# Optimization experiments

Hardware: AMD Instinct MI355X
Metric: run time of the kernel (lower is better)

## Reference

```python
import jax, jax.numpy as jnp
import numpy as np
from jax import lax

B, SEQ, ENC_IN, PRED = 16, 512, 321, 96
DM, DSTATE, DCONV, EXPAND, ELAYERS = 512, 16, 4, 2, 2
DI = EXPAND * DM            # 1024
DTRANK = -(-DM // 16)       # 32
EPS = 1e-5
NMAMBA = 2                  # mamba1/mamba2 shared across all encoder layers


def setup_inputs() -> dict:
    key = jax.random.key(0)
    ks = jax.random.split(key, 10)
    nrm = lambda k, sh, s=0.02: jax.random.normal(k, sh, dtype=jnp.float32) * s
    return {
        "x": jax.random.normal(ks[0], (B, SEQ, ENC_IN), dtype=jnp.float32),
        "revin_w": jnp.ones((ENC_IN,), jnp.float32),
        "revin_b": jnp.zeros((ENC_IN,), jnp.float32),
        "lin1_w": nrm(ks[1], (DM, SEQ)),
        "lin1_b": jnp.zeros((DM,), jnp.float32),
        "head_w": nrm(ks[2], (PRED, DM)),
        "head_b": jnp.zeros((PRED,), jnp.float32),
        "in_proj_w": nrm(ks[3], (NMAMBA, 2 * DI, DM)),
        "conv_w": nrm(ks[4], (NMAMBA, DI, DCONV), 0.1),
        "conv_b": jnp.zeros((NMAMBA, DI), jnp.float32),
        "x_proj_w": nrm(ks[5], (NMAMBA, DTRANK + 2 * DSTATE, DI)),
        "dt_proj_w": nrm(ks[6], (NMAMBA, DI, DTRANK), 0.1),
        "dt_proj_b": nrm(ks[7], (NMAMBA, DI), 0.1),
        "A_log": jnp.log(jnp.broadcast_to(jnp.arange(1, DSTATE + 1, dtype=jnp.float32), (NMAMBA, DI, DSTATE))),
        "D": jnp.ones((NMAMBA, DI), jnp.float32),
        "out_proj_w": nrm(ks[8], (NMAMBA, DM, DI)),
    }


def _mamba(x, ipw, cw, cb, xpw, dpw, dpb, A_log, Dp, opw):
    # x: (B, L, DM) -> (B, L, DM); standard Mamba selective-scan block
    xz = jnp.einsum('bld,ed->ble', x, ipw)            # (B,L,2*DI)
    xr, z = jnp.split(xz, 2, axis=-1)
    # causal depthwise conv over token axis L
    k = cw.T[:, None, :]                              # (DCONV,1,DI)
    xc = lax.conv_general_dilated(xr, k, window_strides=(1,), padding=[(DCONV - 1, 0)],
                                  dimension_numbers=('NHC', 'HIO', 'NHC'), feature_group_count=DI)
    xc = jax.nn.silu(xc + cb)
    dbl = jnp.einsum('bld,ed->ble', xc, xpw)          # (B,L,DTRANK+2N)
    dt, Bm, Cm = jnp.split(dbl, [DTRANK, DTRANK + DSTATE], axis=-1)
    delta = jax.nn.softplus(jnp.einsum('blr,dr->bld', dt, dpw) + dpb)  # (B,L,DI)
    A = -jnp.exp(A_log)                               # (DI,N)

    def step(h, xs):
        d_t, B_t, C_t, x_t = xs                       # (B,DI),(B,N),(B,N),(B,DI)
        dA = jnp.exp(d_t[..., None] * A)              # (B,DI,N)
        h = dA * h + (d_t * x_t)[..., None] * B_t[:, None, :]
        y = jnp.einsum('bdn,bn->bd', h, C_t)
        return h, y

    h0 = jnp.zeros((x.shape[0], DI, DSTATE), x.dtype)
    xs = (delta.transpose(1, 0, 2), Bm.transpose(1, 0, 2), Cm.transpose(1, 0, 2), xc.transpose(1, 0, 2))
    _, ys = lax.scan(step, h0, xs)
    y = ys.transpose(1, 0, 2) + Dp * xc
    y = y * jax.nn.silu(z)
    return jnp.einsum('bld,ed->ble', y, opw)


def reference(x, revin_w, revin_b, lin1_w, lin1_b, head_w, head_b,
              in_proj_w, conv_w, conv_b, x_proj_w, dt_proj_w, dt_proj_b,
              A_log, D, out_proj_w):
    # RevIN normalize (stats over time dim)
    mean = x.mean(1, keepdims=True)
    std = jnp.sqrt(x.var(1, keepdims=True) + EPS)
    xn = (x - mean) / std * revin_w + revin_b
    # channels become tokens; embed lookback window
    t = xn.transpose(0, 2, 1)                         # (B, ENC_IN, SEQ)
    t = t @ lin1_w.T + lin1_b                         # (B, ENC_IN, DM)
    p = lambda i: (in_proj_w[i], conv_w[i], conv_b[i], x_proj_w[i],
                   dt_proj_w[i], dt_proj_b[i], A_log[i], D[i], out_proj_w[i])
    for _ in range(ELAYERS):                          # mamba1/mamba2 weights shared across layers
        fwd = _mamba(t, *p(0))
        bwd = jnp.flip(_mamba(jnp.flip(t, 1), *p(1)), 1)   # is_flip bidirectional branch
        t = fwd + bwd + t
    out = t @ head_w.T + head_b                       # (B, ENC_IN, PRED)
    out = out.transpose(0, 2, 1)                      # (B, PRED, ENC_IN)
    # RevIN denorm
    out = (out - revin_b) / (revin_w + EPS * EPS)
    out = out * std + mean
    return out
```

## Files before the change

kernel.cpp:

```cpp
#include <hip/hip_runtime.h>
#include <hip/hip_bf16.h>
#include <cstdint>
#include <cstddef>

#define B_    16
#define SEQ_  512
#define CIN_  321
#define PRED_ 96
#define DM_   512
#define DI_   1024
#define NST_  16
#define RNK_  32
#define L_    321
#define NT_   (B_*CIN_)
#define PADM_ 5248
#define TC_   41
#define NC_   8
#define PS_   384

typedef unsigned short ushort_t;
typedef __bf16 bf16x8 __attribute__((ext_vector_type(8)));
typedef float  f32x4  __attribute__((ext_vector_type(4)));
typedef __attribute__((address_space(3))) void lds_void_t;
typedef const __attribute__((address_space(1))) void gbl_void_t;

__device__ __forceinline__ float sigmoidf_(float x){ return 1.f/(1.f+__expf(-x)); }
__device__ __forceinline__ float softplusf_(float x){
    return (x > 15.f) ? x : __logf(1.f + __expf(x));
}
__device__ __forceinline__ ushort_t f2bf(float f){
    union { float f; unsigned u; } v; v.f = f;
    unsigned r = v.u + 0x7FFF + ((v.u >> 16) & 1);
    return (ushort_t)(r >> 16);
}
__device__ __forceinline__ float bf2f(ushort_t u){
    return __uint_as_float(((unsigned)u) << 16);
}

struct EpiBiasDual {
    float* C; ushort_t* Cb; const float* bias;
    __device__ void operator()(int z, int m, int n, float v) const {
        float o = v + bias[n];
        C[(size_t)m*DM_ + n] = o;
        Cb[(size_t)m*DM_ + n] = f2bf(o);
    }
};
struct EpiXZ {
    ushort_t* xzb;
    __device__ void operator()(int z, int m, int n, float v) const {
        int mm = m;
        if (z) { int b = m / L_; int l = m - b*L_; mm = b*L_ + (L_-1 - l); }
        xzb[(size_t)z*PADM_*2*DI_ + (size_t)mm*(2*DI_) + n] = f2bf(v);
    }
};
struct EpiDbl {
    float* C; ushort_t* dtb;
    __device__ void operator()(int z, int m, int n, float v) const {
        if (n < 32)
            dtb[(size_t)z*PADM_*32 + (size_t)m*32 + n] = f2bf(v);
        else if (n < 64)
            C[(size_t)z*NT_*64 + (size_t)m*64 + n] = v;
    }
};
struct EpiSpB {
    ushort_t* C; const float* bias;
    __device__ void operator()(int z, int m, int n, float v) const {
        C[(size_t)z*NT_*DI_ + (size_t)m*DI_ + n] = f2bf(softplusf_(v + bias[z*DI_ + n]));
    }
};
struct EpiP {
    float* P;
    __device__ void operator()(int z, int m, int n, float v) const {
        P[(size_t)z*NT_*DM_ + (size_t)m*DM_ + n] = v;
    }
};
struct EpiHead {
    float* out; const float* bias; const float* mean; const float* stdv;
    const float* rw; const float* rb;
    __device__ void operator()(int z, int m, int n, float v) const {
        int b = m / CIN_, c = m - b*CIN_;
        float o = v + bias[n];
        o = (o - rb[c]) / (rw[c] + 1e-10f);
        o = o * stdv[m] + mean[m];
        out[((size_t)b*PRED_ + n)*CIN_ + c] = o;
    }
};

template<int BK, typename Epi>
__global__ __launch_bounds__(256) void gemm_bf16(const ushort_t* __restrict__ A, int lda, size_t zsa,
                                                 const ushort_t* __restrict__ Bw, int ldb, size_t zsb,
                                                 int M, int N, int K, Epi epi)
{
    __shared__ __align__(16) ushort_t As[128*BK];
    __shared__ __align__(16) ushort_t Bs[128*BK];
    const int z = blockIdx.z;
    A += (size_t)z*zsa; Bw += (size_t)z*zsb;
    const int tid  = threadIdx.x;
    const int m0 = blockIdx.x * 128, n0 = blockIdx.y * 128;
    const int wave = tid >> 6, lane = tid & 63;
    const int wm = (wave & 1) * 64, wn = (wave >> 1) * 64;
    const int ln16 = lane & 15, quad = lane >> 4;

    f32x4 acc[4][4] = {};

    if (BK == 64) {
        const int r8 = lane >> 3;
        const int colg = ((lane & 7) ^ r8) * 8;
        const ushort_t* Ag = A + (size_t)(m0 + wave*32 + r8)*lda + colg;
        const ushort_t* Bg = Bw + (size_t)(n0 + wave*32 + r8)*ldb + colg;
        ushort_t* AsW = As + wave*32*64;
        ushort_t* BsW = Bs + wave*32*64;
        for (int k0 = 0; k0 < K; k0 += 64) {
            #pragma unroll
            for (int j = 0; j < 4; ++j) {
                __builtin_amdgcn_global_load_lds((gbl_void_t*)(Ag + k0 + (size_t)(j*8)*lda),
                                                 (lds_void_t*)(AsW + j*8*64), 16, 0, 0);
                __builtin_amdgcn_global_load_lds((gbl_void_t*)(Bg + k0 + (size_t)(j*8)*ldb),
                                                 (lds_void_t*)(BsW + j*8*64), 16, 0, 0);
            }
            __syncthreads();
            #pragma unroll
            for (int ks = 0; ks < 2; ++ks) {
                bf16x8 af[4], bfr[4];
                #pragma unroll
                for (int i = 0; i < 4; ++i) {
                    int ra = wm + i*16 + ln16;
                    af[i]  = *(const bf16x8*)(As + ra*64 + (((ks*4 + quad) ^ (ra & 7)) * 8));
                    int rb2 = wn + i*16 + ln16;
                    bfr[i] = *(const bf16x8*)(Bs + rb2*64 + (((ks*4 + quad) ^ (rb2 & 7)) * 8));
                }
                #pragma unroll
                for (int mi = 0; mi < 4; ++mi)
                    #pragma unroll
                    for (int ni = 0; ni < 4; ++ni)
                        acc[mi][ni] = __builtin_amdgcn_mfma_f32_16x16x32_bf16(af[mi], bfr[ni], acc[mi][ni], 0, 0, 0);
            }
            __syncthreads();
        }
    } else {
        const int srow = lane >> 2, scol = (lane & 3) * 8;
        const ushort_t* Ag = A + (size_t)(m0 + wave*32 + srow)*lda + scol;
        const ushort_t* Bg = Bw + (size_t)(n0 + wave*32 + srow)*ldb + scol;
        ushort_t* AsW = As + wave*32*32;
        ushort_t* BsW = Bs + wave*32*32;
        for (int k0 = 0; k0 < K; k0 += 32) {
            __builtin_amdgcn_global_load_lds((gbl_void_t*)(Ag + k0),                  (lds_void_t*)AsW,           16, 0, 0);
            __builtin_amdgcn_global_load_lds((gbl_void_t*)(Ag + k0 + 16*(size_t)lda), (lds_void_t*)(AsW + 16*32), 16, 0, 0);
            __builtin_amdgcn_global_load_lds((gbl_void_t*)(Bg + k0),                  (lds_void_t*)BsW,           16, 0, 0);
            __builtin_amdgcn_global_load_lds((gbl_void_t*)(Bg + k0 + 16*(size_t)ldb), (lds_void_t*)(BsW + 16*32), 16, 0, 0);
            __syncthreads();
            bf16x8 af[4], bfr[4];
            #pragma unroll
            for (int i = 0; i < 4; ++i)
                af[i] = *(const bf16x8*)(As + (wm + i*16 + ln16)*32 + quad*8);
            #pragma unroll
            for (int i = 0; i < 4; ++i)
                bfr[i] = *(const bf16x8*)(Bs + (wn + i*16 + ln16)*32 + quad*8);
            #pragma unroll
            for (int mi = 0; mi < 4; ++mi)
                #pragma unroll
                for (int ni = 0; ni < 4; ++ni)
                    acc[mi][ni] = __builtin_amdgcn_mfma_f32_16x16x32_bf16(af[mi], bfr[ni], acc[mi][ni], 0, 0, 0);
            __syncthreads();
        }
    }

    #pragma unroll
    for (int mi = 0; mi < 4; ++mi) {
        #pragma unroll
        for (int r = 0; r < 4; ++r) {
            int m = m0 + wm + mi*16 + quad*4 + r;
            if (m >= M) continue;
            #pragma unroll
            for (int ni = 0; ni < 4; ++ni) {
                int n = n0 + wn + ni*16 + ln16;
                if (n < N) epi(z, m, n, acc[mi][ni][r]);
            }
        }
    }
}

struct CvtArgs {
    const float* src[7];
    ushort_t*    dst[7];
    int n4[7];
    int start[8];
};
__global__ __launch_bounds__(256) void cvt_all(CvtArgs a)
{
    int bid = blockIdx.x;
    int seg = 0;
    #pragma unroll
    for (int i = 0; i < 6; ++i) seg += (bid >= a.start[i+1]) ? 1 : 0;
    int idx = (bid - a.start[seg])*256 + threadIdx.x;
    if (idx < a.n4[seg]) {
        float4 v = ((const float4*)a.src[seg])[idx];
        ushort4 u; u.x=f2bf(v.x); u.y=f2bf(v.y); u.z=f2bf(v.z); u.w=f2bf(v.w);
        ((ushort4*)a.dst[seg])[idx] = u;
    }
}

__global__ __launch_bounds__(256) void revin_partial(const float* __restrict__ x,
                                                     float* __restrict__ psum,
                                                     float* __restrict__ psq)
{
    int b = blockIdx.x;
    int c0 = blockIdx.y * 64;
    int sz = blockIdx.z;
    int cl = threadIdx.x & 63;
    int sl = threadIdx.x >> 6;
    int c = c0 + cl;
    int s0 = sz * 64;
    float sum = 0.f, sq = 0.f;
    if (c < CIN_) {
        #pragma unroll
        for (int i = 0; i < 16; ++i) {
            int s = s0 + sl + i*4;
            float v = x[((size_t)b*SEQ_ + s)*CIN_ + c];
            sum += v; sq += v*v;
        }
    }
    __shared__ float ssum[4][64], ssq[4][64];
    ssum[sl][cl] = sum; ssq[sl][cl] = sq;
    __syncthreads();
    if (sl == 0 && c < CIN_) {
        float s = ssum[0][cl]+ssum[1][cl]+ssum[2][cl]+ssum[3][cl];
        float q = ssq[0][cl]+ssq[1][cl]+ssq[2][cl]+ssq[3][cl];
        psum[((size_t)b*8 + sz)*PS_ + c] = s;
        psq [((size_t)b*8 + sz)*PS_ + c] = q;
    }
}
__global__ __launch_bounds__(384) void revin_final(const float* __restrict__ psum,
                                                   const float* __restrict__ psq,
                                                   float* __restrict__ meanb,
                                                   float* __restrict__ stdb)
{
    int b = blockIdx.x;
    int c = threadIdx.x;
    if (c >= CIN_) return;
    float s = 0.f, q = 0.f;
    #pragma unroll
    for (int i = 0; i < 8; ++i) {
        s += psum[((size_t)b*8 + i)*PS_ + c];
        q += psq [((size_t)b*8 + i)*PS_ + c];
    }
    float mn = s * (1.f/SEQ_);
    float var = q * (1.f/SEQ_) - mn*mn;
    meanb[b*CIN_ + c] = mn;
    stdb[b*CIN_ + c]  = sqrtf(var + 1e-5f);
}

__global__ __launch_bounds__(256) void norm_transpose(const float* __restrict__ x,
                                                      const float* __restrict__ meanb,
                                                      const float* __restrict__ stdb,
                                                      const float* __restrict__ rw,
                                                      const float* __restrict__ rb,
                                                      ushort_t* __restrict__ xt)
{
    __shared__ float tile[64][65];
    int b = blockIdx.x, s0 = blockIdx.y*64, c0 = blockIdx.z*64;
    int cl = threadIdx.x & 63, sl = threadIdx.x >> 6;
    #pragma unroll
    for (int i = 0; i < 16; ++i) {
        int s = s0 + sl + i*4;
        int c = c0 + cl;
        float v = 0.f;
        if (c < CIN_) v = x[((size_t)b*SEQ_ + s)*CIN_ + c];
        tile[sl + i*4][cl] = v;
    }
    __syncthreads();
    int sl2 = threadIdx.x & 63, cl2 = threadIdx.x >> 6;
    #pragma unroll
    for (int i = 0; i < 16; ++i) {
        int c = c0 + cl2 + i*4;
        if (c >= CIN_) continue;
        int m = b*CIN_ + c;
        float v = tile[sl2][cl2 + i*4];
        v = (v - meanb[m]) / stdb[m] * rw[c] + rb[c];
        xt[(size_t)m*SEQ_ + s0 + sl2] = f2bf(v);
    }
}

__global__ __launch_bounds__(256) void conv_silu(const ushort_t* __restrict__ xzb,
                                                 const float* __restrict__ cw,
                                                 const float* __restrict__ cb,
                                                 ushort_t* __restrict__ xcb)
{
    int m = blockIdx.x;
    int d = blockIdx.y*256 + threadIdx.x;
    int im = blockIdx.z;
    const ushort_t* xz = xzb + (size_t)im*PADM_*2*DI_;
    int b = m / L_, l = m - b*L_;
    float4 w = ((const float4*)cw)[(size_t)im*DI_ + d];
    float wv[4] = {w.x, w.y, w.z, w.w};
    float a = cb[im*DI_ + d];
    #pragma unroll
    for (int j = 0; j < 4; ++j) {
        int ls = l - 3 + j;
        if (ls >= 0) a += bf2f(xz[((size_t)(b*L_ + ls))*(2*DI_) + d]) * wv[j];
    }
    float o = a * sigmoidf_(a);
    xcb[(size_t)im*PADM_*DI_ + (size_t)m*DI_ + d] = f2bf(o);
}

#define SCAN_LOADS(tok)                                                          \
    float dv = bf2f(dlz[(size_t)(tok)*DI_ + d]);                                 \
    float xv = bf2f(xcz[(size_t)(tok)*DI_ + d]);                                 \
    float4 B0 = *(const float4*)(dbz + (size_t)(tok)*64 + 32);                   \
    float4 B1 = *(const float4*)(dbz + (size_t)(tok)*64 + 36);                   \
    float4 B2 = *(const float4*)(dbz + (size_t)(tok)*64 + 40);                   \
    float4 B3 = *(const float4*)(dbz + (size_t)(tok)*64 + 44);                   \
    float Bv[16] = {B0.x,B0.y,B0.z,B0.w, B1.x,B1.y,B1.z,B1.w,                    \
                    B2.x,B2.y,B2.z,B2.w, B3.x,B3.y,B3.z,B3.w};

__global__ __launch_bounds__(64, 1) void scan_p1(const ushort_t* __restrict__ dl,
                                                 const ushort_t* __restrict__ xcb,
                                                 const float* __restrict__ dbl,
                                                 const float* __restrict__ A_log,
                                                 float* __restrict__ hloc,
                                                 float* __restrict__ Ssum)
{
    const int im = blockIdx.z >> 4, b = blockIdx.z & 15;
    const int c = blockIdx.y;
    const int d = blockIdx.x*64 + threadIdx.x;
    const ushort_t* dlz = dl + (size_t)im*NT_*DI_;
    const ushort_t* xcz = xcb + (size_t)im*PADM_*DI_;
    const float* dbz = dbl + (size_t)im*NT_*64;
    float a[NST_];
    #pragma unroll
    for (int n = 0; n < NST_; ++n)
        a[n] = -__expf(A_log[((size_t)im*DI_ + d)*NST_ + n]);
    bool uni = true;
    #pragma unroll
    for (int n = 1; n < NST_; ++n)
        uni = uni && (fabsf(a[n] - (n+1)*a[0]) <= 1e-3f*(n+1));
    const float a0 = a[0];
    const int t0 = c*TC_, tend = (t0 + TC_ < L_) ? t0 + TC_ : L_;
    float h[NST_] = {};
    float S = 0.f;
    if (uni) {
        for (int t = t0; t < tend; ++t) {
            int tok = b*L_ + t;
            SCAN_LOADS(tok)
            S += dv;
            float du = dv * xv;
            float e1 = __expf(dv * a0), dAn = e1;
            #pragma unroll
            for (int n = 0; n < NST_; ++n) { h[n] = dAn*h[n] + du*Bv[n]; dAn *= e1; }
        }
    } else {
        for (int t = t0; t < tend; ++t) {
            int tok = b*L_ + t;
            SCAN_LOADS(tok)
            S += dv;
            float du = dv * xv;
            #pragma unroll
            for (int n = 0; n < NST_; ++n) h[n] = __expf(dv*a[n])*h[n] + du*Bv[n];
        }
    }
    size_t base = ((size_t)(im*16 + b)*NC_ + c);
    Ssum[base*DI_ + d] = S;
    #pragma unroll
    for (int n = 0; n < NST_; ++n)
        hloc[(base*NST_ + n)*DI_ + d] = h[n];
}

__global__ __launch_bounds__(64, 1) void scan_compose(const float* __restrict__ A_log,
                                                      float* __restrict__ hloc,
                                                      const float* __restrict__ Ssum)
{
    const int im = blockIdx.z >> 4, b = blockIdx.z & 15;
    const int d = blockIdx.x*64 + threadIdx.x;
    float a[NST_];
    #pragma unroll
    for (int n = 0; n < NST_; ++n)
        a[n] = -__expf(A_log[((size_t)im*DI_ + d)*NST_ + n]);
    float carry[NST_] = {};
    for (int c = 0; c < NC_; ++c) {
        size_t base = ((size_t)(im*16 + b)*NC_ + c);
        float S = Ssum[base*DI_ + d];
        #pragma unroll
        for (int n = 0; n < NST_; ++n) {
            size_t idx = (base*NST_ + n)*DI_ + d;
            float hl = hloc[idx];
            hloc[idx] = carry[n];
            carry[n] = __expf(a[n]*S)*carry[n] + hl;
        }
    }
}

__global__ __launch_bounds__(64, 1) void scan_p2(const ushort_t* __restrict__ dl,
                                                 const ushort_t* __restrict__ xcb,
                                                 ushort_t* __restrict__ xzb,
                                                 const float* __restrict__ dbl,
                                                 const float* __restrict__ A_log,
                                                 const float* __restrict__ Dp,
                                                 const float* __restrict__ hloc)
{
    const int im = blockIdx.z >> 4, b = blockIdx.z & 15;
    const int c = blockIdx.y;
    const int d = blockIdx.x*64 + threadIdx.x;
    const ushort_t* dlz = dl + (size_t)im*NT_*DI_;
    const ushort_t* xcz = xcb + (size_t)im*PADM_*DI_;
    const float* dbz = dbl + (size_t)im*NT_*64;
    ushort_t* xzz = xzb + (size_t)im*PADM_*2*DI_;
    float a[NST_];
    #pragma unroll
    for (int n = 0; n < NST_; ++n)
        a[n] = -__expf(A_log[((size_t)im*DI_ + d)*NST_ + n]);
    bool uni = true;
    #pragma unroll
    for (int n = 1; n < NST_; ++n)
        uni = uni && (fabsf(a[n] - (n+1)*a[0]) <= 1e-3f*(n+1));
    const float a0 = a[0];
    const float Dd = Dp[im*DI_ + d];
    const int t0 = c*TC_, tend = (t0 + TC_ < L_) ? t0 + TC_ : L_;
    size_t base = ((size_t)(im*16 + b)*NC_ + c);
    float h[NST_];
    #pragma unroll
    for (int n = 0; n < NST_; ++n)
        h[n] = hloc[(base*NST_ + n)*DI_ + d];
    if (uni) {
        for (int t = t0; t < tend; ++t) {
            int tok = b*L_ + t;
            SCAN_LOADS(tok)
            float4 C0 = *(const float4*)(dbz + (size_t)tok*64 + 48);
            float4 C1 = *(const float4*)(dbz + (size_t)tok*64 + 52);
            float4 C2 = *(const float4*)(dbz + (size_t)tok*64 + 56);
            float4 C3 = *(const float4*)(dbz + (size_t)tok*64 + 60);
            float Cv[16] = {C0.x,C0.y,C0.z,C0.w, C1.x,C1.y,C1.z,C1.w,
                            C2.x,C2.y,C2.z,C2.w, C3.x,C3.y,C3.z,C3.w};
            float zg = bf2f(xzz[(size_t)tok*2*DI_ + DI_ + d]);
            float du = dv * xv;
            float y = 0.f;
            float e1 = __expf(dv * a0), dAn = e1;
            #pragma unroll
            for (int n = 0; n < NST_; ++n) {
                h[n] = dAn*h[n] + du*Bv[n];
                y += h[n]*Cv[n];
                dAn *= e1;
            }
            y = (y + Dd*xv) * (zg * sigmoidf_(zg));
            xzz[(size_t)tok*2*DI_ + d] = f2bf(y);
        }
    } else {
        for (int t = t0; t < tend; ++t) {
            int tok = b*L_ + t;
            SCAN_LOADS(tok)
            float4 C0 = *(const float4*)(dbz + (size_t)tok*64 + 48);
            float4 C1 = *(const float4*)(dbz + (size_t)tok*64 + 52);
            float4 C2 = *(const float4*)(dbz + (size_t)tok*64 + 56);
            float4 C3 = *(const float4*)(dbz + (size_t)tok*64 + 60);
            float Cv[16] = {C0.x,C0.y,C0.z,C0.w, C1.x,C1.y,C1.z,C1.w,
                            C2.x,C2.y,C2.z,C2.w, C3.x,C3.y,C3.z,C3.w};
            float zg = bf2f(xzz[(size_t)tok*2*DI_ + DI_ + d]);
            float du = dv * xv;
            float y = 0.f;
            #pragma unroll
            for (int n = 0; n < NST_; ++n) {
                h[n] = __expf(dv*a[n])*h[n] + du*Bv[n];
                y += h[n]*Cv[n];
            }
            y = (y + Dd*xv) * (zg * sigmoidf_(zg));
            xzz[(size_t)tok*2*DI_ + d] = f2bf(y);
        }
    }
}

__global__ __launch_bounds__(256) void fuse_res(float* __restrict__ t,
                                                ushort_t* __restrict__ tbf,
                                                const float* __restrict__ P)
{
    const int row4 = DM_/4;
    size_t i = (size_t)blockIdx.x*256 + threadIdx.x;
    int m = (int)(i / row4), c4 = (int)(i - (size_t)m*row4);
    int b = m / L_, l = m - b*L_;
    int mf = b*L_ + (L_-1 - l);
    float4 tv = ((float4*)t)[i];
    float4 p0 = ((const float4*)P)[(size_t)m*row4 + c4];
    float4 p1 = ((const float4*)(P + (size_t)NT_*DM_))[(size_t)mf*row4 + c4];
    tv.x += p0.x + p1.x; tv.y += p0.y + p1.y;
    tv.z += p0.z + p1.z; tv.w += p0.w + p1.w;
    ((float4*)t)[i] = tv;
    ushort4 u; u.x=f2bf(tv.x); u.y=f2bf(tv.y); u.z=f2bf(tv.z); u.w=f2bf(tv.w);
    ((ushort4*)tbf)[i] = u;
}

extern "C" void kernel_launch(void* const* d_in, const int* in_sizes, int n_in,
                              void* d_out, int out_size, void* d_ws, size_t ws_size,
                              hipStream_t stream)
{
    const float* x      = (const float*)d_in[0];
    const float* rw     = (const float*)d_in[1];
    const float* rb     = (const float*)d_in[2];
    const float* lin1_w = (const float*)d_in[3];
    const float* lin1_b = (const float*)d_in[4];
    const float* head_w = (const float*)d_in[5];
    const float* head_b = (const float*)d_in[6];
    const float* ipw    = (const float*)d_in[7];
    const float* cw     = (const float*)d_in[8];
    const float* cb     = (const float*)d_in[9];
    const float* xpw    = (const float*)d_in[10];
    const float* dpw    = (const float*)d_in[11];
    const float* dpb    = (const float*)d_in[12];
    const float* A_log  = (const float*)d_in[13];
    const float* Dp     = (const float*)d_in[14];
    const float* opw    = (const float*)d_in[15];
    float* out = (float*)d_out;

    float* ws = (float*)d_ws;
    size_t off = 0;
    auto alloc = [&](size_t nfloats) { float* p = ws + off; off += (nfloats + 63) & ~(size_t)63; return p; };
    float* meanb = alloc(NT_);
    float* stdb  = alloc(NT_);
    float* psum  = alloc((size_t)B_*8*PS_);
    float* psq   = alloc((size_t)B_*8*PS_);
    ushort_t* xnt_bf = (ushort_t*)alloc((size_t)PADM_*SEQ_/2);
    ushort_t* tbf    = (ushort_t*)alloc((size_t)PADM_*DM_/2);
    float* tres  = alloc((size_t)NT_*DM_);
    ushort_t* xzb = (ushort_t*)alloc((size_t)2*PADM_*2*DI_/2);
    ushort_t* xcb = (ushort_t*)alloc((size_t)2*PADM_*DI_/2);
    float* dl    = alloc((size_t)2*NT_*DI_);
    float* dblb  = alloc((size_t)2*NT_*64);
    ushort_t* dtb = (ushort_t*)alloc((size_t)2*PADM_*32/2);
    float* hloc  = alloc((size_t)2*16*NC_*NST_*DI_);
    float* Ssum  = alloc((size_t)2*16*NC_*DI_);
    ushort_t* lin1_bf = (ushort_t*)alloc((size_t)DM_*SEQ_/2);
    ushort_t* head_bf = (ushort_t*)alloc((size_t)128*DM_/2);
    ushort_t* ipw_bf  = (ushort_t*)alloc((size_t)2*2*DI_*DM_/2);
    ushort_t* opw_bf  = (ushort_t*)alloc((size_t)2*DM_*DI_/2);
    ushort_t* xpw_bf  = (ushort_t*)alloc((size_t)2*128*DI_/2);
    ushort_t* dpw_bf  = (ushort_t*)alloc((size_t)2*DI_*RNK_/2);
    ushort_t* dlb = (ushort_t*)dl;
    (void)ws_size; (void)in_sizes; (void)n_in; (void)out_size;

    dim3 blk(256);

    CvtArgs ca;
    const float* srcs[7] = {lin1_w, head_w, ipw, opw, dpw, xpw, xpw + 64*DI_};
    ushort_t*    dsts[7] = {lin1_bf, head_bf, ipw_bf, opw_bf, dpw_bf, xpw_bf, xpw_bf + 128*DI_};
    int ns[7] = {DM_*SEQ_, PRED_*DM_, 2*2*DI_*DM_, 2*DM_*DI_, 2*DI_*RNK_, 64*DI_, 64*DI_};
    ca.start[0] = 0;
    for (int i = 0; i < 7; ++i) {
        ca.src[i] = srcs[i]; ca.dst[i] = dsts[i]; ca.n4[i] = ns[i]/4;
        ca.start[i+1] = ca.start[i] + (ca.n4[i] + 255)/256;
    }
    cvt_all<<<dim3(ca.start[7]), blk, 0, stream>>>(ca);

    revin_partial<<<dim3(B_, 6, 8), blk, 0, stream>>>(x, psum, psq);
    revin_final<<<dim3(B_), dim3(384), 0, stream>>>(psum, psq, meanb, stdb);
    norm_transpose<<<dim3(B_, 8, 6), blk, 0, stream>>>(x, meanb, stdb, rw, rb, xnt_bf);
    gemm_bf16<64><<<dim3(41, 4, 1), blk, 0, stream>>>(xnt_bf, SEQ_, 0, lin1_bf, SEQ_, 0,
                                                      NT_, DM_, SEQ_,
                                                      EpiBiasDual{tres, tbf, lin1_b});

    for (int layer = 0; layer < 2; ++layer) {
        gemm_bf16<64><<<dim3(41, 16, 2), blk, 0, stream>>>(
            tbf, DM_, 0, ipw_bf, DM_, (size_t)2*DI_*DM_,
            NT_, 2*DI_, DM_, EpiXZ{xzb});
        conv_silu<<<dim3(NT_, 4, 2), blk, 0, stream>>>(xzb, cw, cb, xcb);
        gemm_bf16<64><<<dim3(41, 1, 2), blk, 0, stream>>>(
            xcb, DI_, (size_t)PADM_*DI_, xpw_bf, DI_, (size_t)128*DI_,
            NT_, 64, DI_, EpiDbl{dblb, dtb});
        gemm_bf16<32><<<dim3(41, 8, 2), blk, 0, stream>>>(
            dtb, 32, (size_t)PADM_*32, dpw_bf, 32, (size_t)DI_*RNK_,
            NT_, DI_, RNK_, EpiSpB{dlb, dpb});
        scan_p1<<<dim3(16, NC_, 32), dim3(64), 0, stream>>>(dlb, xcb, dblb, A_log, hloc, Ssum);
        scan_compose<<<dim3(16, 1, 32), dim3(64), 0, stream>>>(A_log, hloc, Ssum);
        scan_p2<<<dim3(16, NC_, 32), dim3(64), 0, stream>>>(dlb, xcb, xzb, dblb, A_log, Dp, hloc);
        gemm_bf16<64><<<dim3(41, 4, 2), blk, 0, stream>>>(
            xzb, 2*DI_, (size_t)PADM_*2*DI_, opw_bf, DI_, (size_t)DM_*DI_,
            NT_, DM_, DI_, EpiP{dl});
        fuse_res<<<dim3((NT_*DM_/4)/256), blk, 0, stream>>>(tres, tbf, dl);
    }
    gemm_bf16<64><<<dim3(41, 1, 1), blk, 0, stream>>>(tbf, DM_, 0, head_bf, DM_, 0,
                                                      NT_, PRED_, DM_,
                                                      EpiHead{out, head_b, meanb, stdb, rw, rb});
}
```

Before: 611.0 us.

## Fold scan carry composition into scan_p2, vectorize conv, store out_proj in bf16

Removes the separate scan_compose kernel: each scan_p2 block now rebuilds its incoming state by folding the prefix of chunk-local states, using a geometric power trick when A is uniform. This saves one launch and a serial pass, at the cost of redundant prefix work in later chunks. conv_silu is rewritten so each thread handles four channels with vectorized loads and stores, and the out_proj GEMM writes bf16 instead of fp32 to halve that buffer's traffic into fuse_res. Writing bf16 there adds rounding error to the residual update.

```diff
diff --git a/kernel.cpp b/kernel.cpp
--- a/kernel.cpp
+++ b/kernel.cpp
@@ -69,9 +69,9 @@
     }
 };
 struct EpiP {
-    float* P;
+    ushort_t* P;
     __device__ void operator()(int z, int m, int n, float v) const {
-        P[(size_t)z*NT_*DM_ + (size_t)m*DM_ + n] = v;
+        P[(size_t)z*NT_*DM_ + (size_t)m*DM_ + n] = f2bf(v);
     }
 };
 struct EpiHead {
@@ -287,20 +287,35 @@
                                                  ushort_t* __restrict__ xcb)
 {
     int m = blockIdx.x;
-    int d = blockIdx.y*256 + threadIdx.x;
-    int im = blockIdx.z;
+    int im = blockIdx.y;
+    int d4 = threadIdx.x * 4;
     const ushort_t* xz = xzb + (size_t)im*PADM_*2*DI_;
     int b = m / L_, l = m - b*L_;
-    float4 w = ((const float4*)cw)[(size_t)im*DI_ + d];
-    float wv[4] = {w.x, w.y, w.z, w.w};
-    float a = cb[im*DI_ + d];
+    float wjt[4][4];
     #pragma unroll
     for (int j = 0; j < 4; ++j) {
-        int ls = l - 3 + j;
-        if (ls >= 0) a += bf2f(xz[((size_t)(b*L_ + ls))*(2*DI_) + d]) * wv[j];
-    }
-    float o = a * sigmoidf_(a);
-    xcb[(size_t)im*PADM_*DI_ + (size_t)m*DI_ + d] = f2bf(o);
+        float4 w = ((const float4*)cw)[(size_t)im*DI_ + d4 + j];
+        wjt[j][0]=w.x; wjt[j][1]=w.y; wjt[j][2]=w.z; wjt[j][3]=w.w;
+    }
+    float4 bb = *(const float4*)(cb + (size_t)im*DI_ + d4);
+    float acc4[4] = {bb.x, bb.y, bb.z, bb.w};
+    #pragma unroll
+    for (int t = 0; t < 4; ++t) {
+        int ls = l - 3 + t;
+        if (ls >= 0) {
+            ushort4 xv = *(const ushort4*)(xz + (size_t)(b*L_ + ls)*2*DI_ + d4);
+            acc4[0] += bf2f(xv.x) * wjt[0][t];
+            acc4[1] += bf2f(xv.y) * wjt[1][t];
+            acc4[2] += bf2f(xv.z) * wjt[2][t];
+            acc4[3] += bf2f(xv.w) * wjt[3][t];
+        }
+    }
+    ushort4 o;
+    o.x = f2bf(acc4[0] * sigmoidf_(acc4[0]));
+    o.y = f2bf(acc4[1] * sigmoidf_(acc4[1]));
+    o.z = f2bf(acc4[2] * sigmoidf_(acc4[2]));
+    o.w = f2bf(acc4[3] * sigmoidf_(acc4[3]));
+    *(ushort4*)(xcb + (size_t)im*PADM_*DI_ + (size_t)m*DI_ + d4) = o;
 }
 
 #define SCAN_LOADS(tok)                                                          \
@@ -365,37 +380,14 @@
         hloc[(base*NST_ + n)*DI_ + d] = h[n];
 }
 
-__global__ __launch_bounds__(64, 1) void scan_compose(const float* __restrict__ A_log,
-                                                      float* __restrict__ hloc,
-                                                      const float* __restrict__ Ssum)
-{
-    const int im = blockIdx.z >> 4, b = blockIdx.z & 15;
-    const int d = blockIdx.x*64 + threadIdx.x;
-    float a[NST_];
-    #pragma unroll
-    for (int n = 0; n < NST_; ++n)
-        a[n] = -__expf(A_log[((size_t)im*DI_ + d)*NST_ + n]);
-    float carry[NST_] = {};
-    for (int c = 0; c < NC_; ++c) {
-        size_t base = ((size_t)(im*16 + b)*NC_ + c);
-        float S = Ssum[base*DI_ + d];
-        #pragma unroll
-        for (int n = 0; n < NST_; ++n) {
-            size_t idx = (base*NST_ + n)*DI_ + d;
-            float hl = hloc[idx];
-            hloc[idx] = carry[n];
-            carry[n] = __expf(a[n]*S)*carry[n] + hl;
-        }
-    }
-}
-
 __global__ __launch_bounds__(64, 1) void scan_p2(const ushort_t* __restrict__ dl,
                                                  const ushort_t* __restrict__ xcb,
                                                  ushort_t* __restrict__ xzb,
                                                  const float* __restrict__ dbl,
                                                  const float* __restrict__ A_log,
                                                  const float* __restrict__ Dp,
-                                                 const float* __restrict__ hloc)
+                                                 const float* __restrict__ hloc,
+                                                 const float* __restrict__ Ssum)
 {
     const int im = blockIdx.z >> 4, b = blockIdx.z & 15;
     const int c = blockIdx.y;
@@ -415,11 +407,26 @@
     const float a0 = a[0];
     const float Dd = Dp[im*DI_ + d];
     const int t0 = c*TC_, tend = (t0 + TC_ < L_) ? t0 + TC_ : L_;
-    size_t base = ((size_t)(im*16 + b)*NC_ + c);
-    float h[NST_];
-    #pragma unroll
-    for (int n = 0; n < NST_; ++n)
-        h[n] = hloc[(base*NST_ + n)*DI_ + d];
+    const size_t gbase = (size_t)(im*16 + b)*NC_;
+
+    float h[NST_] = {};
+    for (int cc = 0; cc < c; ++cc) {
+        size_t base2 = gbase + cc;
+        float S = Ssum[base2*DI_ + d];
+        if (uni) {
+            float eS = __expf(S * a0), ef = eS;
+            #pragma unroll
+            for (int n = 0; n < NST_; ++n) {
+                h[n] = ef*h[n] + hloc[(base2*NST_ + n)*DI_ + d];
+                ef *= eS;
+            }
+        } else {
+            #pragma unroll
+            for (int n = 0; n < NST_; ++n)
+                h[n] = __expf(S*a[n])*h[n] + hloc[(base2*NST_ + n)*DI_ + d];
+        }
+    }
+
     if (uni) {
         for (int t = t0; t < tend; ++t) {
             int tok = b*L_ + t;
@@ -469,7 +476,7 @@
 
 __global__ __launch_bounds__(256) void fuse_res(float* __restrict__ t,
                                                 ushort_t* __restrict__ tbf,
-                                                const float* __restrict__ P)
+                                                const ushort_t* __restrict__ P)
 {
     const int row4 = DM_/4;
     size_t i = (size_t)blockIdx.x*256 + threadIdx.x;
@@ -477,10 +484,12 @@
     int b = m / L_, l = m - b*L_;
     int mf = b*L_ + (L_-1 - l);
     float4 tv = ((float4*)t)[i];
-    float4 p0 = ((const float4*)P)[(size_t)m*row4 + c4];
-    float4 p1 = ((const float4*)(P + (size_t)NT_*DM_))[(size_t)mf*row4 + c4];
-    tv.x += p0.x + p1.x; tv.y += p0.y + p1.y;
-    tv.z += p0.z + p1.z; tv.w += p0.w + p1.w;
+    ushort4 p0 = ((const ushort4*)P)[(size_t)m*row4 + c4];
+    ushort4 p1 = ((const ushort4*)(P + (size_t)NT_*DM_))[(size_t)mf*row4 + c4];
+    tv.x += bf2f(p0.x) + bf2f(p1.x);
+    tv.y += bf2f(p0.y) + bf2f(p1.y);
+    tv.z += bf2f(p0.z) + bf2f(p1.z);
+    tv.w += bf2f(p0.w) + bf2f(p1.w);
     ((float4*)t)[i] = tv;
     ushort4 u; u.x=f2bf(tv.x); u.y=f2bf(tv.y); u.z=f2bf(tv.z); u.w=f2bf(tv.w);
     ((ushort4*)tbf)[i] = u;
@@ -532,6 +541,7 @@
     ushort_t* xpw_bf  = (ushort_t*)alloc((size_t)2*128*DI_/2);
     ushort_t* dpw_bf  = (ushort_t*)alloc((size_t)2*DI_*RNK_/2);
     ushort_t* dlb = (ushort_t*)dl;
+    ushort_t* Pb  = (ushort_t*)dl;
     (void)ws_size; (void)in_sizes; (void)n_in; (void)out_size;
 
     dim3 blk(256);
@@ -558,7 +568,7 @@
         gemm_bf16<64><<<dim3(41, 16, 2), blk, 0, stream>>>(
             tbf, DM_, 0, ipw_bf, DM_, (size_t)2*DI_*DM_,
             NT_, 2*DI_, DM_, EpiXZ{xzb});
-        conv_silu<<<dim3(NT_, 4, 2), blk, 0, stream>>>(xzb, cw, cb, xcb);
+        conv_silu<<<dim3(NT_, 2), blk, 0, stream>>>(xzb, cw, cb, xcb);
         gemm_bf16<64><<<dim3(41, 1, 2), blk, 0, stream>>>(
             xcb, DI_, (size_t)PADM_*DI_, xpw_bf, DI_, (size_t)128*DI_,
             NT_, 64, DI_, EpiDbl{dblb, dtb});
@@ -566,12 +576,11 @@
             dtb, 32, (size_t)PADM_*32, dpw_bf, 32, (size_t)DI_*RNK_,
             NT_, DI_, RNK_, EpiSpB{dlb, dpb});
         scan_p1<<<dim3(16, NC_, 32), dim3(64), 0, stream>>>(dlb, xcb, dblb, A_log, hloc, Ssum);
-        scan_compose<<<dim3(16, 1, 32), dim3(64), 0, stream>>>(A_log, hloc, Ssum);
-        scan_p2<<<dim3(16, NC_, 32), dim3(64), 0, stream>>>(dlb, xcb, xzb, dblb, A_log, Dp, hloc);
+        scan_p2<<<dim3(16, NC_, 32), dim3(64), 0, stream>>>(dlb, xcb, xzb, dblb, A_log, Dp, hloc, Ssum);
         gemm_bf16<64><<<dim3(41, 4, 2), blk, 0, stream>>>(
             xzb, 2*DI_, (size_t)PADM_*2*DI_, opw_bf, DI_, (size_t)DM_*DI_,
-            NT_, DM_, DI_, EpiP{dl});
-        fuse_res<<<dim3((NT_*DM_/4)/256), blk, 0, stream>>>(tres, tbf, dl);
+            NT_, DM_, DI_, EpiP{Pb});
+        fuse_res<<<dim3((NT_*DM_/4)/256), blk, 0, stream>>>(tres, tbf, Pb);
     }
     gemm_bf16<64><<<dim3(41, 1, 1), blk, 0, stream>>>(tbf, DM_, 0, head_bf, DM_, 0,
                                                       NT_, PRED_, DM_,
```

Measured after the change: 607.1 us. Within noise of the previous version (-0.6%).
